# Kernel optimization log

Measured on AMD Instinct MI355X. Metric: run time of the kernel, lower is better.

## Reference

```python
import jax, jax.numpy as jnp
import numpy as np

B, C, H, W = 64, 512, 32, 32


def _conv1x1(x, w):
    # x: [B,C,H,W], w: [Cout,Cin] (1x1 conv kernel squeezed) -> [B,Cout,H,W]
    return jnp.einsum('bchw,oc->bohw', x, w)


def _spike(v, threshold):
    # Single-timestep LIF with fresh state: mem = decay*0 + v = v; fire where mem >= threshold.
    # Binary spike output (membrane reset after fire is irrelevant for one step).
    return (v >= threshold).astype(v.dtype)


def setup_inputs() -> dict:
    key = jax.random.key(0)
    ks = jax.random.split(key, 5)
    xavier = 1.0 / np.sqrt(C)  # xavier_normal std for square 1x1 conv: sqrt(2/(C+C))
    return {
        'x': jax.random.normal(ks[0], (B, C, H, W), dtype=jnp.float32),
        'w_sieve1': jax.random.normal(ks[1], (C, C), dtype=jnp.float32) * xavier,
        'w_sieve2': jax.random.normal(ks[2], (C, C), dtype=jnp.float32) * xavier,
        'w_source': jax.random.normal(ks[3], (C, C), dtype=jnp.float32) * xavier,
        'w_lin': jax.random.normal(ks[4], (C, C), dtype=jnp.float32) * xavier,
    }


def reference(x, w_sieve1, w_sieve2, w_source, w_lin):
    # lif_input called with threshold override = 1
    x_in = _spike(x, 1.0)                               # binary spikes [B,C,H,W]
    x_res = x_in
    source = _spike(_conv1x1(x_in, w_source), 1.0)      # lif_source, threshold=1.0 (min=0 clamp inert: 1.0>0)
    sieve = _spike(_conv1x1(x_in, w_sieve1) + _conv1x1(x_in, w_sieve2), 4.0)  # lif_Sieve, threshold=4.0
    gated = sieve * source                              # spike-gated activation
    out = (_conv1x1(gated, w_lin) + x_res) * 0.5
    return out
```

## Files before the change

kernel.cpp:

```cpp
#include <hip/hip_runtime.h>
#include <hip/hip_bf16.h>

#define WL_CAP 65536u

typedef __attribute__((ext_vector_type(4))) int i32x4;

__global__ void prep_wsum_i8(const float* __restrict__ w1, const float* __restrict__ w2,
                             char* __restrict__ wsum) {
  int i = (blockIdx.x * 256 + threadIdx.x) * 4;
  float4 a = *reinterpret_cast<const float4*>(w1 + i);
  float4 b = *reinterpret_cast<const float4*>(w2 + i);
  int v0 = __float2int_rn(fminf(fmaxf((a.x + b.x) * 256.f, -127.f), 127.f));
  int v1 = __float2int_rn(fminf(fmaxf((a.y + b.y) * 256.f, -127.f), 127.f));
  int v2 = __float2int_rn(fminf(fmaxf((a.z + b.z) * 256.f, -127.f), 127.f));
  int v3 = __float2int_rn(fminf(fmaxf((a.w + b.w) * 256.f, -127.f), 127.f));
  unsigned u = (v0 & 0xFF) | ((v1 & 0xFF) << 8) | ((v2 & 0xFF) << 16) | ((v3 & 0xFF) << 24);
  *reinterpret_cast<unsigned*>(wsum + i) = u;
}

__global__ __launch_bounds__(256) void spike_pack(const float* __restrict__ x,
                                                  float* __restrict__ out,
                                                  unsigned* __restrict__ xinb) {
  __shared__ unsigned char sp[64 * 132];
  int bx = blockIdx.x;
  int ht = bx & 7;
  int ct = (bx >> 3) & 7;
  int b = bx >> 6;
  int hw0 = ht * 128, c0 = ct * 64;
  int t = threadIdx.x;
  int hw4 = (t & 31) * 4;
  int crow = t >> 5;
  size_t base = ((size_t)(b * 512 + c0)) * 1024 + hw0;
#pragma unroll
  for (int pass = 0; pass < 8; ++pass) {
    int c_l = crow + pass * 8;
    size_t g = base + (size_t)c_l * 1024 + hw4;
    float4 v = *reinterpret_cast<const float4*>(x + g);
    unsigned s0 = (v.x >= 1.f) ? 1u : 0u;
    unsigned s1 = (v.y >= 1.f) ? 1u : 0u;
    unsigned s2 = (v.z >= 1.f) ? 1u : 0u;
    unsigned s3 = (v.w >= 1.f) ? 1u : 0u;
    float4 ov = make_float4(0.5f * (float)s0, 0.5f * (float)s1,
                            0.5f * (float)s2, 0.5f * (float)s3);
    *reinterpret_cast<float4*>(out + g) = ov;
    *reinterpret_cast<unsigned*>(&sp[c_l * 132 + hw4]) =
        s0 | (s1 << 8) | (s2 << 16) | (s3 << 24);
  }
  __syncthreads();
  int px = t >> 1, half = t & 1;
  unsigned bits = 0;
#pragma unroll
  for (int j = 0; j < 32; ++j)
    bits |= ((unsigned)sp[(half * 32 + j) * 132 + px]) << j;
  xinb[(size_t)ct * 131072 + (size_t)(b * 1024 + hw0 + px) * 2 + half] = bits;
}

__global__ __launch_bounds__(256) void gemm_fire_i8(const char* __restrict__ wsum,
                                                    const unsigned short* __restrict__ xinb,
                                                    unsigned* __restrict__ counter,
                                                    unsigned* __restrict__ wl) {
  __shared__ char As[128 * 512];
  int m0 = blockIdx.x * 128;
  int n0 = blockIdx.y * 128;
  int t = threadIdx.x;
  int lane = t & 63;
  int wv = t >> 6;
  int wr = wv >> 1, wc = wv & 1;
  int fr = lane & 15;
  int kgrp = lane >> 4;

#pragma unroll
  for (int i = 0; i < 16; ++i) {
    int idx = t + i * 256;
    int row = idx >> 5;
    int col16 = (idx & 31) * 16;
    int scol = col16 ^ ((row & 7) << 4);
    const char* ga = wsum + (size_t)(m0 + row) * 512 + scol;
    __builtin_amdgcn_global_load_lds((const __attribute__((address_space(1))) void*)ga,
                                     (__attribute__((address_space(3))) void*)(As + idx * 16),
                                     16, 0, 0);
  }

  unsigned short bbits[4][8];
#pragma unroll
  for (int ni = 0; ni < 4; ++ni) {
    int prow = n0 + wc * 64 + ni * 16 + fr;
    const unsigned short* pb = xinb + (size_t)prow * 4 + kgrp;
#pragma unroll
    for (int kt = 0; kt < 8; ++kt) bbits[ni][kt] = pb[(size_t)kt * 262144];
  }

  i32x4 acc[4][4];
#pragma unroll
  for (int i = 0; i < 4; ++i)
#pragma unroll
    for (int j = 0; j < 4; ++j) acc[i][j] = (i32x4){0, 0, 0, 0};

  __syncthreads();

#pragma unroll
  for (int kt = 0; kt < 8; ++kt) {
    i32x4 av[4];
#pragma unroll
    for (int mi = 0; mi < 4; ++mi) {
      int row = wr * 64 + mi * 16 + fr;
      int col = (kt * 64 + kgrp * 16) ^ ((row & 7) << 4);
      av[mi] = *reinterpret_cast<const i32x4*>(&As[row * 512 + col]);
    }
#pragma unroll
    for (int ni = 0; ni < 4; ++ni) {
      unsigned s = bbits[ni][kt];
      i32x4 bv;
      bv[0] = (int)((((s      ) & 0xFu) * 0x00204081u) & 0x01010101u);
      bv[1] = (int)((((s >>  4) & 0xFu) * 0x00204081u) & 0x01010101u);
      bv[2] = (int)((((s >>  8) & 0xFu) * 0x00204081u) & 0x01010101u);
      bv[3] = (int)((((s >> 12) & 0xFu) * 0x00204081u) & 0x01010101u);
#pragma unroll
      for (int mi = 0; mi < 4; ++mi)
        acc[mi][ni] = __builtin_amdgcn_mfma_i32_16x16x64_i8(av[mi], bv, acc[mi][ni], 0, 0, 0);
    }
  }

  int rowg = (lane >> 4) * 4;
#pragma unroll
  for (int mi = 0; mi < 4; ++mi)
#pragma unroll
    for (int ni = 0; ni < 4; ++ni)
#pragma unroll
      for (int v = 0; v < 4; ++v) {
        if (acc[mi][ni][v] >= 896) {
          unsigned o = (unsigned)(m0 + wr * 64 + mi * 16 + rowg + v);
          unsigned p = (unsigned)(n0 + wc * 64 + ni * 16 + fr);
          unsigned slot = atomicAdd(counter, 1u);
          if (slot < WL_CAP) wl[slot] = (o << 16) | p;
        }
      }
}

__global__ void finish_fires(const float* __restrict__ x, const float* __restrict__ w1,
                             const float* __restrict__ w2, const float* __restrict__ wsrc,
                             const float* __restrict__ wlin, float* __restrict__ out,
                             const unsigned* __restrict__ counter,
                             const unsigned* __restrict__ wl) {
  unsigned n = *counter;
  if (n > WL_CAP) n = WL_CAP;
  for (unsigned i = blockIdx.x * blockDim.x + threadIdx.x; i < n;
       i += gridDim.x * blockDim.x) {
    unsigned e = wl[i];
    int o = (int)(e >> 16);
    int p = (int)(e & 0xFFFFu);
    int b = p >> 10, hw = p & 1023;
    const float* xb = x + (size_t)b * 512 * 1024 + hw;
    float s1 = 0.f, s2 = 0.f;
    for (int c = 0; c < 512; ++c) {
      if (xb[(size_t)c * 1024] >= 1.f) {
        s1 += w1[o * 512 + c] + w2[o * 512 + c];
        s2 += wsrc[o * 512 + c];
      }
    }
    if (s1 >= 4.0f && s2 >= 1.0f) {
      for (int c = 0; c < 512; ++c)
        atomicAdd(&out[((size_t)b * 512 + c) * 1024 + hw], 0.5f * wlin[c * 512 + o]);
    }
  }
}

__global__ void fallback_dense(const float* __restrict__ x, const float* __restrict__ w1,
                               const float* __restrict__ w2, const float* __restrict__ wsrc,
                               const float* __restrict__ wlin, float* __restrict__ out) {
  __shared__ float xin[512];
  __shared__ float gated[512];
  int p = blockIdx.x;
  int b = p >> 10, hw = p & 1023;
  const float* xb = x + (size_t)b * 512 * 1024 + hw;
  for (int c = threadIdx.x; c < 512; c += 256)
    xin[c] = (xb[(size_t)c * 1024] >= 1.f) ? 1.f : 0.f;
  __syncthreads();
  for (int o = threadIdx.x; o < 512; o += 256) {
    float s1 = 0.f, s2 = 0.f;
    for (int c = 0; c < 512; ++c) {
      float xv = xin[c];
      s1 += xv * (w1[o * 512 + c] + w2[o * 512 + c]);
      s2 += xv * wsrc[o * 512 + c];
    }
    gated[o] = (s1 >= 4.f && s2 >= 1.f) ? 1.f : 0.f;
  }
  __syncthreads();
  for (int c = threadIdx.x; c < 512; c += 256) {
    float a = 0.f;
    for (int o = 0; o < 512; ++o) a += gated[o] * wlin[c * 512 + o];
    out[((size_t)b * 512 + c) * 1024 + hw] = 0.5f * (a + xin[c]);
  }
}

extern "C" void kernel_launch(void* const* d_in, const int* in_sizes, int n_in,
                              void* d_out, int out_size, void* d_ws, size_t ws_size,
                              hipStream_t stream) {
  const float* x    = (const float*)d_in[0];
  const float* w1   = (const float*)d_in[1];
  const float* w2   = (const float*)d_in[2];
  const float* wsrc = (const float*)d_in[3];
  const float* wlin = (const float*)d_in[4];
  float* out = (float*)d_out;

  const size_t NEED = (size_t)8 * 1024 * 1024;
  if (ws_size >= NEED) {
    unsigned* counter = (unsigned*)d_ws;
    unsigned* wl = (unsigned*)((char*)d_ws + 1024);
    char* wsum_i8 = (char*)d_ws + (1u << 20);
    unsigned* xinb = (unsigned*)((char*)d_ws + (2u << 20));

    hipMemsetAsync(d_ws, 0, 4, stream);
    prep_wsum_i8<<<256, 256, 0, stream>>>(w1, w2, wsum_i8);
    spike_pack<<<4096, 256, 0, stream>>>(x, out, xinb);
    gemm_fire_i8<<<dim3(4, 512), 256, 0, stream>>>(wsum_i8, (const unsigned short*)xinb,
                                                   counter, wl);
    finish_fires<<<dim3(32), 64, 0, stream>>>(x, w1, w2, wsrc, wlin, out, counter, wl);
  } else {
    fallback_dense<<<65536, 256, 0, stream>>>(x, w1, w2, wsrc, wlin, out);
  }
}
```

Measured before the change: 85.30 us.

## Pack spike bits directly per 16-channel group without LDS transpose

Replaces the LDS-transpose spike packing kernel with one where each thread reads 16 channels for 4 pixels and builds 16-bit masks in registers. This removes shared memory use and the barrier. The bit-packed layout changes to [channel-group][pixel] uint16, and the GEMM's B-fragment load indexing is updated to match. Output and mask stores now use nontemporal hints to avoid polluting cache with the large streaming writes.

```diff
diff --git a/kernel.cpp b/kernel.cpp
--- a/kernel.cpp
+++ b/kernel.cpp
@@ -4,6 +4,8 @@
 #define WL_CAP 65536u
 
 typedef __attribute__((ext_vector_type(4))) int i32x4;
+typedef __attribute__((ext_vector_type(4))) float f32x4v;
+typedef __attribute__((ext_vector_type(4))) unsigned short u16x4v;
 
 __global__ void prep_wsum_i8(const float* __restrict__ w1, const float* __restrict__ w2,
                              char* __restrict__ wsum) {
@@ -18,45 +20,38 @@
   *reinterpret_cast<unsigned*>(wsum + i) = u;
 }
 
-__global__ __launch_bounds__(256) void spike_pack(const float* __restrict__ x,
-                                                  float* __restrict__ out,
-                                                  unsigned* __restrict__ xinb) {
-  __shared__ unsigned char sp[64 * 132];
-  int bx = blockIdx.x;
-  int ht = bx & 7;
-  int ct = (bx >> 3) & 7;
-  int b = bx >> 6;
-  int hw0 = ht * 128, c0 = ct * 64;
+__global__ __launch_bounds__(256) void spike_pack_direct(const float* __restrict__ x,
+                                                         float* __restrict__ out,
+                                                         unsigned short* __restrict__ xinb16) {
   int t = threadIdx.x;
-  int hw4 = (t & 31) * 4;
-  int crow = t >> 5;
-  size_t base = ((size_t)(b * 512 + c0)) * 1024 + hw0;
-#pragma unroll
-  for (int pass = 0; pass < 8; ++pass) {
-    int c_l = crow + pass * 8;
-    size_t g = base + (size_t)c_l * 1024 + hw4;
-    float4 v = *reinterpret_cast<const float4*>(x + g);
+  int g = blockIdx.x;
+  int b = g >> 5, cg = g & 31;
+  int px = t * 4;
+  size_t rowbase = ((size_t)(b * 512 + cg * 16)) * 1024 + (size_t)px;
+  unsigned u0 = 0, u1 = 0, u2 = 0, u3 = 0;
+#pragma unroll 4
+  for (int ci = 0; ci < 16; ++ci) {
+    size_t gaddr = rowbase + (size_t)ci * 1024;
+    f32x4v v = *reinterpret_cast<const f32x4v*>(x + gaddr);
     unsigned s0 = (v.x >= 1.f) ? 1u : 0u;
     unsigned s1 = (v.y >= 1.f) ? 1u : 0u;
     unsigned s2 = (v.z >= 1.f) ? 1u : 0u;
     unsigned s3 = (v.w >= 1.f) ? 1u : 0u;
-    float4 ov = make_float4(0.5f * (float)s0, 0.5f * (float)s1,
-                            0.5f * (float)s2, 0.5f * (float)s3);
-    *reinterpret_cast<float4*>(out + g) = ov;
-    *reinterpret_cast<unsigned*>(&sp[c_l * 132 + hw4]) =
-        s0 | (s1 << 8) | (s2 << 16) | (s3 << 24);
-  }
-  __syncthreads();
-  int px = t >> 1, half = t & 1;
-  unsigned bits = 0;
-#pragma unroll
-  for (int j = 0; j < 32; ++j)
-    bits |= ((unsigned)sp[(half * 32 + j) * 132 + px]) << j;
-  xinb[(size_t)ct * 131072 + (size_t)(b * 1024 + hw0 + px) * 2 + half] = bits;
+    f32x4v ov;
+    ov.x = 0.5f * (float)s0; ov.y = 0.5f * (float)s1;
+    ov.z = 0.5f * (float)s2; ov.w = 0.5f * (float)s3;
+    __builtin_nontemporal_store(ov, reinterpret_cast<f32x4v*>(out + gaddr));
+    u0 |= s0 << ci; u1 |= s1 << ci; u2 |= s2 << ci; u3 |= s3 << ci;
+  }
+  u16x4v o;
+  o.x = (unsigned short)u0; o.y = (unsigned short)u1;
+  o.z = (unsigned short)u2; o.w = (unsigned short)u3;
+  __builtin_nontemporal_store(o, reinterpret_cast<u16x4v*>(
+      xinb16 + (size_t)cg * 65536 + (size_t)(b * 1024 + px)));
 }
 
 __global__ __launch_bounds__(256) void gemm_fire_i8(const char* __restrict__ wsum,
-                                                    const unsigned short* __restrict__ xinb,
+                                                    const unsigned short* __restrict__ xinb16,
                                                     unsigned* __restrict__ counter,
                                                     unsigned* __restrict__ wl) {
   __shared__ char As[128 * 512];
@@ -85,9 +80,9 @@
 #pragma unroll
   for (int ni = 0; ni < 4; ++ni) {
     int prow = n0 + wc * 64 + ni * 16 + fr;
-    const unsigned short* pb = xinb + (size_t)prow * 4 + kgrp;
-#pragma unroll
-    for (int kt = 0; kt < 8; ++kt) bbits[ni][kt] = pb[(size_t)kt * 262144];
+#pragma unroll
+    for (int kt = 0; kt < 8; ++kt)
+      bbits[ni][kt] = xinb16[(size_t)(kt * 4 + kgrp) * 65536 + prow];
   }
 
   i32x4 acc[4][4];
@@ -208,13 +203,12 @@
     unsigned* counter = (unsigned*)d_ws;
     unsigned* wl = (unsigned*)((char*)d_ws + 1024);
     char* wsum_i8 = (char*)d_ws + (1u << 20);
-    unsigned* xinb = (unsigned*)((char*)d_ws + (2u << 20));
-
-    hipMemsetAsync(d_ws, 0, 4, stream);
+    unsigned short* xinb16 = (unsigned short*)((char*)d_ws + (2u << 20));
+
+    (void)hipMemsetAsync(d_ws, 0, 4, stream);
     prep_wsum_i8<<<256, 256, 0, stream>>>(w1, w2, wsum_i8);
-    spike_pack<<<4096, 256, 0, stream>>>(x, out, xinb);
-    gemm_fire_i8<<<dim3(4, 512), 256, 0, stream>>>(wsum_i8, (const unsigned short*)xinb,
-                                                   counter, wl);
+    spike_pack_direct<<<2048, 256, 0, stream>>>(x, out, xinb16);
+    gemm_fire_i8<<<dim3(4, 512), 256, 0, stream>>>(wsum_i8, xinb16, counter, wl);
     finish_fires<<<dim3(32), 64, 0, stream>>>(x, w1, w2, wsrc, wlin, out, counter, wl);
   } else {
     fallback_dense<<<65536, 256, 0, stream>>>(x, w1, w2, wsrc, wlin, out);
```

After: 77.24 us. 9.4% less time.
